# Optimization experiments

Hardware: AMD Instinct MI355X
Metric: run time of the kernel (lower is better)

The kernel has to match this reference:

```python
import jax, jax.numpy as jnp
import numpy as np

B, N, D, R, W, H, I = 256, 2048, 128, 4, 1, 1024, 1024
CI = I + R * D                       # controller input size (1536)
IF = 2 * D * W + 2 * W + 1 + 4 * R + D * R   # interface size (787)
OPI = H + R * D                      # output_proj input (1536)


def _norm(v):
    # F.normalize(dim=-1): x / max(||x||, eps)
    return v / jnp.maximum(jnp.linalg.norm(v, axis=-1, keepdims=True), 1e-12)


def setup_inputs() -> dict:
    key = jax.random.key(0)
    ks = jax.random.split(key, 16)
    u = lambda k, shape, fan: jax.random.uniform(k, shape, jnp.float32, -1.0 / np.sqrt(fan), 1.0 / np.sqrt(fan))
    return {
        "x": jax.random.normal(ks[0], (B, I), jnp.float32),
        "memory": jax.random.normal(ks[1], (N, D), jnp.float32) * np.sqrt(2.0 / (N + D)),  # xavier-ish
        "usage": jax.random.uniform(ks[2], (N,), jnp.float32),          # usage in [0,1)
        "link": jax.random.normal(ks[3], (N, N), jnp.float32) * 0.01,   # non-trivial link state
        "W_ih": u(ks[4], (4 * H, CI), H),
        "W_hh": u(ks[5], (4 * H, H), H),
        "b_ih": u(ks[6], (4 * H,), H),
        "b_hh": u(ks[7], (4 * H,), H),
        "W_if": u(ks[8], (IF, H), H),
        "b_if": u(ks[9], (IF,), H),
        "W_out": u(ks[10], (H, OPI), OPI),
        "b_out": u(ks[11], (H,), OPI),
    }


def reference(x, memory, usage, link, W_ih, W_hh, b_ih, b_hh, W_if, b_if, W_out, b_out):
    # initial uniform read weights (prev state at first step)
    prev_rw = jnp.full((B, R, N), 1.0 / N, x.dtype)
    read_flat = (prev_rw @ memory).reshape(B, -1)                 # (B, R*D)
    cin = jnp.concatenate([x, read_flat], axis=-1)                # (B, CI)

    # single LSTM step, h0 = c0 = 0, torch gate order i,f,g,o
    g = cin @ W_ih.T + b_ih + b_hh
    gi, gf, gg, go = jnp.split(g, 4, axis=-1)
    c = jax.nn.sigmoid(gi) * jnp.tanh(gg)
    h = jax.nn.sigmoid(go) * jnp.tanh(c)                          # (B, H) controller out

    itf = h @ W_if.T + b_if                                       # (B, IF)
    o = 0
    write_vals = itf[:, o:o + D * W].reshape(B, W, D); o += D * W
    erase = jax.nn.sigmoid(itf[:, o:o + D * W]).reshape(B, W, D); o += D * W
    write_gates = jax.nn.sigmoid(itf[:, o:o + W]); o += W         # (B, W)
    alloc_gate = jax.nn.sigmoid(itf[:, o:o + 1]); o += 1          # (B, 1)
    o += W                                                        # free gates (parsed, unused)
    read_modes = jax.nn.softmax(itf[:, o:o + 3 * R].reshape(B, R, 3), -1); o += 3 * R
    read_str = jax.nn.softplus(itf[:, o:o + R]); o += R           # (B, R)
    read_keys = itf[:, o:o + D * R].reshape(B, R, D)

    # content addressing for the write (strength = 1)
    mem_n = _norm(memory)
    cw = jax.nn.softmax(_norm(write_vals.mean(1)) @ mem_n.T, -1)  # (B, N)

    # allocation weighting: sorted-usage cumprod (per source semantics)
    idx = jnp.argsort(usage)
    su = usage[idx]
    cp = jnp.cumprod(1.0 - su)
    alloc_s = jnp.concatenate([su[:1], su[1:] * cp[:-1]])
    alloc = jnp.zeros_like(usage).at[idx].set(alloc_s)[None, :] * alloc_gate  # (B, N)

    write_w = write_gates[:, :, None] * (0.5 * cw + 0.5 * alloc)[:, None, :]  # (B, W, N)

    # temporal link update: batch-mean of diag-masked outer product, decay 0.9
    lu = jnp.einsum('bwn,bwm->nm', write_w, write_w) / B
    lu = lu * (1.0 - jnp.eye(N, dtype=lu.dtype))
    link_new = link * 0.9 + lu * 0.1

    # memory write (erase then add, batch-mean)
    ev = erase * write_gates[:, :, None]
    av = write_vals * write_gates[:, :, None]
    erase_mat = jnp.einsum('bwn,bwd->nd', write_w, ev) / B
    add_mat = jnp.einsum('bwn,bwd->nd', write_w, av) / B
    mem_new = memory * (1.0 - erase_mat) + add_mat

    # read addressing on updated memory and updated link (all R heads vectorized)
    sim = jnp.einsum('brd,nd->brn', _norm(read_keys), _norm(mem_new))
    content_r = jax.nn.softmax(sim * read_str[:, :, None], -1)    # (B, R, N)
    backward_w = jnp.einsum('brn,nm->brm', prev_rw, link_new)     # mode 1: prev @ L
    forward_w = jnp.einsum('brn,mn->brm', prev_rw, link_new)      # mode 2: prev @ L^T
    new_rw = (read_modes[..., 0:1] * content_r
              + read_modes[..., 1:2] * backward_w
              + read_modes[..., 2:3] * forward_w)                 # (B, R, N)

    read_out = (new_rw @ mem_new).reshape(B, -1)                  # (B, R*D)
    out = jnp.concatenate([h, read_out], axis=-1) @ W_out.T + b_out
    return out
```

## Files before the change

### kernel.cpp

```cpp
#include <hip/hip_runtime.h>
#include <cmath>

#define DEVI __device__ __forceinline__

DEVI float sigm(float x){ return 1.f/(1.f+expf(-x)); }

typedef __attribute__((ext_vector_type(8))) _Float16 half8;
typedef __attribute__((ext_vector_type(4))) _Float16 half4;
typedef __attribute__((ext_vector_type(4))) float float4v;


__global__ void k_zero(float* __restrict__ p, int n){
  int i = blockIdx.x*256 + threadIdx.x;
  if (i < n) p[i] = 0.f;
}

__global__ __launch_bounds__(256) void k_stage1(
    const float* __restrict__ mem, float* __restrict__ cm, _Float16* __restrict__ mem_h)
{
  __shared__ float smem[4][132];
  const int blk = blockIdx.x, t = threadIdx.x;
  const int wv = t >> 6, lane = t & 63;
  int rbase = blk*16 + wv*4;
  float x0[4], x1[4], ss[4];
  #pragma unroll
  for (int u = 0; u < 4; u++){
    const float* a = mem + (size_t)(rbase+u)*128;
    x0[u] = a[lane]; x1[u] = a[lane+64];
  }
  #pragma unroll
  for (int u = 0; u < 4; u++) ss[u] = x0[u]*x0[u] + x1[u]*x1[u];
  #pragma unroll
  for (int o = 1; o < 64; o <<= 1){
    #pragma unroll
    for (int u = 0; u < 4; u++) ss[u] += __shfl_xor(ss[u], o);
  }
  float c0 = 0.f, c1 = 0.f;
  #pragma unroll
  for (int u = 0; u < 4; u++){
    float invn = 1.f / fmaxf(sqrtf(ss[u]), 1e-12f);
    mem_h[(size_t)(rbase+u)*128 + lane]      = (_Float16)(x0[u]*invn);
    mem_h[(size_t)(rbase+u)*128 + 64 + lane] = (_Float16)(x1[u]*invn);
    c0 += x0[u]; c1 += x1[u];
  }
  smem[wv][lane] = c0; smem[wv][64+lane] = c1;
  __syncthreads();
  if (t < 128) atomicAdd(&cm[t], smem[0][t]+smem[1][t]+smem[2][t]+smem[3][t]);
}

#define QA 264
#define QB 520
#define QB3 776

template<typename TB> struct BReg;
template<> struct BReg<_Float16>{
  half8 v;
  DEVI void load(const _Float16* p){ v = *(const half8*)p; }
  DEVI half8 get() const { return v; }
};
template<> struct BReg<float>{
  float4v a, b;
  DEVI void load(const float* p){ a = *(const float4v*)p; b = *(const float4v*)(p+4); }
  DEVI half8 get() const {
    half8 h;
    #pragma unroll
    for (int j = 0; j < 4; j++){ h[j] = (_Float16)a[j]; h[4+j] = (_Float16)b[j]; }
    return h;
  }
};

struct ARegX {
  float4v a, b; float sc;
  DEVI void load(const float* __restrict__ x, const float* __restrict__ cm, int row, int k){
    const float* p;
    if (k < 1024){ p = x + (size_t)row*1024 + k; sc = 1.f; }
    else         { p = cm + ((k - 1024) & 127); sc = (1.f/2048.f); }
    a = *(const float4v*)p; b = *(const float4v*)(p+4);
  }
  DEVI half8 get() const {
    half8 h;
    #pragma unroll
    for (int j = 0; j < 4; j++){ h[j] = (_Float16)(a[j]*sc); h[4+j] = (_Float16)(b[j]*sc); }
    return h;
  }
};

template<typename TB>
__global__ __launch_bounds__(256) void gemm_t(
    const _Float16* __restrict__ A, const TB* __restrict__ Bm, float* __restrict__ C,
    int M, int N, int K,
    const float* __restrict__ bias1, const float* __restrict__ bias2)
{
  __shared__ _Float16 Ah[2][8*QA];
  __shared__ _Float16 Bh[2][8*QB];
  const int tid = threadIdx.x;
  const int m0 = blockIdx.y*32, n0 = blockIdx.x*64;
  const int T = K >> 6;
  const int arow = tid >> 3, aq = tid & 7;
  const int brow = tid >> 3, bq = tid & 7;
  int nB0 = n0 + brow;      if (nB0 >= N) nB0 = N - 1;
  int nB1 = n0 + brow + 32; if (nB1 >= N) nB1 = N - 1;
  const _Float16* Aptr = A + (size_t)(m0 + arow)*K + aq*8;
  const TB* Bp0 = Bm + (size_t)nB0*K + bq*8;
  const TB* Bp1 = Bm + (size_t)nB1*K + bq*8;
  const int wA  = aq*QA + arow*8;
  const int wB0 = bq*QB + brow*8;
  const int wB1 = bq*QB + (brow+32)*8;
  const int wv_ = tid >> 6, lane = tid & 63;
  const int fq = lane >> 4, fr = lane & 15;
  const int m16 = (wv_ & 1)*16, nb = (wv_ >> 1)*32;

  half8 ra0, ra1;
  BReg<TB> rb00, rb10, rb01, rb11;
  ra0 = *(const half8*)(Aptr);
  rb00.load(Bp0); rb10.load(Bp1);
  if (T > 1){
    ra1 = *(const half8*)(Aptr + 64);
    rb01.load(Bp0 + 64); rb11.load(Bp1 + 64);
  }
  *(half8*)&Ah[0][wA]  = ra0;
  *(half8*)&Bh[0][wB0] = rb00.get();
  *(half8*)&Bh[0][wB1] = rb10.get();
  __syncthreads();

  float4v acc0 = {0.f,0.f,0.f,0.f}, acc1 = {0.f,0.f,0.f,0.f};
  for (int t = 0; t < T; t++){
    const int cur = t & 1, nxt = cur ^ 1;
    if (t+2 < T){
      if (cur == 0){
        ra0 = *(const half8*)(Aptr + (t+2)*64);
        rb00.load(Bp0 + (t+2)*64); rb10.load(Bp1 + (t+2)*64);
      } else {
        ra1 = *(const half8*)(Aptr + (t+2)*64);
        rb01.load(Bp0 + (t+2)*64); rb11.load(Bp1 + (t+2)*64);
      }
    }
    #pragma unroll
    for (int s = 0; s < 2; s++){
      int q = s*4 + fq;
      half8 a  = *(half8*)&Ah[cur][q*QA + (m16+fr)*8];
      half8 b0 = *(half8*)&Bh[cur][q*QB + (nb+fr)*8];
      half8 b1 = *(half8*)&Bh[cur][q*QB + (nb+16+fr)*8];
      acc0 = __builtin_amdgcn_mfma_f32_16x16x32_f16(a, b0, acc0, 0, 0, 0);
      acc1 = __builtin_amdgcn_mfma_f32_16x16x32_f16(a, b1, acc1, 0, 0, 0);
    }
    if (t+1 < T){
      if (nxt == 1){
        *(half8*)&Ah[1][wA]  = ra1;
        *(half8*)&Bh[1][wB0] = rb01.get();
        *(half8*)&Bh[1][wB1] = rb11.get();
      } else {
        *(half8*)&Ah[0][wA]  = ra0;
        *(half8*)&Bh[0][wB0] = rb00.get();
        *(half8*)&Bh[0][wB1] = rb10.get();
      }
    }
    __syncthreads();
  }

  const int colA = n0 + nb + fr, colB = colA + 16;
  #pragma unroll
  for (int i = 0; i < 4; i++){
    int m = m0 + m16 + fq*4 + i;
    if (colA < N){
      float v = acc0[i];
      if (bias1) v += bias1[colA];
      if (bias2) v += bias2[colA];
      C[(size_t)m*N + colA] = v;
    }
    if (colB < N){
      float v = acc1[i];
      if (bias1) v += bias1[colB];
      if (bias2) v += bias2[colB];
      C[(size_t)m*N + colB] = v;
    }
  }
}

__global__ __launch_bounds__(256) void gemm_hro(
    const _Float16* __restrict__ Ah_, const _Float16* __restrict__ Aro,
    const float* __restrict__ Bm, float* __restrict__ C,
    const float* __restrict__ bias1)
{
  __shared__ _Float16 Ah[2][8*QA];
  __shared__ _Float16 Bh[2][8*QB];
  const int tid = threadIdx.x;
  const int m0 = blockIdx.y*32, n0 = blockIdx.x*64;
  const int T = 24;
  const int arow = tid >> 3, aq = tid & 7;
  const int brow = tid >> 3, bq = tid & 7;
  const int arw = m0 + arow;
  const float* Bp0 = Bm + (size_t)(n0 + brow)*1536 + bq*8;
  const float* Bp1 = Bm + (size_t)(n0 + brow + 32)*1536 + bq*8;
  const int wA  = aq*QA + arow*8;
  const int wB0 = bq*QB + brow*8;
  const int wB1 = bq*QB + (brow+32)*8;
  const int wv_ = tid >> 6, lane = tid & 63;
  const int fq = lane >> 4, fr = lane & 15;
  const int m16 = (wv_ & 1)*16, nb = (wv_ >> 1)*32;

  auto ldA = [&](int k) -> half8 {
    const _Float16* p = (k < 1024) ? (Ah_ + (size_t)arw*1024 + k)
                                   : (Aro + (size_t)arw*512 + (k - 1024));
    return *(const half8*)p;
  };

  half8 ra0, ra1;
  BReg<float> rb00, rb10, rb01, rb11;
  ra0 = ldA(aq*8);
  rb00.load(Bp0); rb10.load(Bp1);
  ra1 = ldA(aq*8 + 64);
  rb01.load(Bp0 + 64); rb11.load(Bp1 + 64);
  *(half8*)&Ah[0][wA]  = ra0;
  *(half8*)&Bh[0][wB0] = rb00.get();
  *(half8*)&Bh[0][wB1] = rb10.get();
  __syncthreads();

  float4v acc0 = {0.f,0.f,0.f,0.f}, acc1 = {0.f,0.f,0.f,0.f};
  for (int t = 0; t < T; t++){
    const int cur = t & 1, nxt = cur ^ 1;
    if (t+2 < T){
      if (cur == 0){
        ra0 = ldA(aq*8 + (t+2)*64);
        rb00.load(Bp0 + (t+2)*64); rb10.load(Bp1 + (t+2)*64);
      } else {
        ra1 = ldA(aq*8 + (t+2)*64);
        rb01.load(Bp0 + (t+2)*64); rb11.load(Bp1 + (t+2)*64);
      }
    }
    #pragma unroll
    for (int s = 0; s < 2; s++){
      int q = s*4 + fq;
      half8 a  = *(half8*)&Ah[cur][q*QA + (m16+fr)*8];
      half8 b0 = *(half8*)&Bh[cur][q*QB + (nb+fr)*8];
      half8 b1 = *(half8*)&Bh[cur][q*QB + (nb+16+fr)*8];
      acc0 = __builtin_amdgcn_mfma_f32_16x16x32_f16(a, b0, acc0, 0, 0, 0);
      acc1 = __builtin_amdgcn_mfma_f32_16x16x32_f16(a, b1, acc1, 0, 0, 0);
    }
    if (t+1 < T){
      if (nxt == 1){
        *(half8*)&Ah[1][wA]  = ra1;
        *(half8*)&Bh[1][wB0] = rb01.get();
        *(half8*)&Bh[1][wB1] = rb11.get();
      } else {
        *(half8*)&Ah[0][wA]  = ra0;
        *(half8*)&Bh[0][wB0] = rb00.get();
        *(half8*)&Bh[0][wB1] = rb10.get();
      }
    }
    __syncthreads();
  }

  const int colA = n0 + nb + fr, colB = colA + 16;
  #pragma unroll
  for (int i = 0; i < 4; i++){
    int m = m0 + m16 + fq*4 + i;
    C[(size_t)m*1024 + colA] = acc0[i] + bias1[colA];
    C[(size_t)m*1024 + colB] = acc1[i] + bias1[colB];
  }
}

__global__ __launch_bounds__(256) void k_gemm_wwExp(
    const _Float16* __restrict__ A, const _Float16* __restrict__ Bm,
    float* __restrict__ C, float* __restrict__ rsum)
{
  __shared__ _Float16 Ah[2][8*QA];
  __shared__ _Float16 Bh[2][8*QB];
  const int tid = threadIdx.x;
  const int m0 = blockIdx.y*32, n0 = blockIdx.x*64;
  const int arow = tid >> 3, aq = tid & 7;
  const int brow = tid >> 3, bq = tid & 7;
  const _Float16* Aptr = A + (size_t)(m0 + arow)*128 + aq*8;
  const _Float16* Bp0 = Bm + (size_t)(n0 + brow)*128 + bq*8;
  const _Float16* Bp1 = Bm + (size_t)(n0 + brow + 32)*128 + bq*8;
  const int wA  = aq*QA + arow*8;
  const int wB0 = bq*QB + brow*8;
  const int wB1 = bq*QB + (brow+32)*8;
  const int wv_ = tid >> 6, lane = tid & 63;
  const int fq = lane >> 4, fr = lane & 15;
  const int m16 = (wv_ & 1)*16, nb = (wv_ >> 1)*32;

  half8 ra  = *(const half8*)(Aptr);
  half8 rb0 = *(const half8*)(Bp0);
  half8 rb1 = *(const half8*)(Bp1);
  *(half8*)&Ah[0][wA]  = ra;
  *(half8*)&Bh[0][wB0] = rb0;
  *(half8*)&Bh[0][wB1] = rb1;
  __syncthreads();

  float4v acc0 = {0.f,0.f,0.f,0.f}, acc1 = {0.f,0.f,0.f,0.f};
  for (int t = 0; t < 2; t++){
    const int cur = t & 1, nxt = cur ^ 1;
    if (t == 0){
      ra  = *(const half8*)(Aptr + 64);
      rb0 = *(const half8*)(Bp0 + 64);
      rb1 = *(const half8*)(Bp1 + 64);
    }
    #pragma unroll
    for (int s = 0; s < 2; s++){
      int q = s*4 + fq;
      half8 a  = *(half8*)&Ah[cur][q*QA + (m16+fr)*8];
      half8 b0 = *(half8*)&Bh[cur][q*QB + (nb+fr)*8];
      half8 b1 = *(half8*)&Bh[cur][q*QB + (nb+16+fr)*8];
      acc0 = __builtin_amdgcn_mfma_f32_16x16x32_f16(a, b0, acc0, 0, 0, 0);
      acc1 = __builtin_amdgcn_mfma_f32_16x16x32_f16(a, b1, acc1, 0, 0, 0);
    }
    if (t == 0){
      *(half8*)&Ah[nxt][wA]  = ra;
      *(half8*)&Bh[nxt][wB0] = rb0;
      *(half8*)&Bh[nxt][wB1] = rb1;
    }
    __syncthreads();
  }

  const int colA = n0 + nb + fr, colB = colA + 16;
  #pragma unroll
  for (int i = 0; i < 4; i++){
    int m = m0 + m16 + fq*4 + i;
    float e0 = expf(acc0[i]);
    float e1 = expf(acc1[i]);
    C[(size_t)m*2048 + colA] = e0;
    C[(size_t)m*2048 + colB] = e1;
    float rs = e0 + e1;
    #pragma unroll
    for (int o = 1; o < 16; o <<= 1) rs += __shfl_xor(rs, o);
    if (fr == 0) atomicAdd(&rsum[m], rs);
  }
}

__global__ __launch_bounds__(256) void k_big2(
    const float* __restrict__ x, const float* __restrict__ cm,
    const float* __restrict__ W,
    const float* __restrict__ b_ih, const float* __restrict__ b_hh,
    _Float16* __restrict__ h,
    const float* __restrict__ usage, float* __restrict__ alloc,
    const float* __restrict__ link, float* __restrict__ rsl, float* __restrict__ cslp)
{
  extern __shared__ char smraw[];
  const int blk = blockIdx.x, tid = threadIdx.x;
  const int wv = tid >> 6, lane = tid & 63;

  if (blk < 256){
    _Float16* AhP = (_Float16*)smraw;
    _Float16* BhP = (_Float16*)(smraw + 2*8*QA*sizeof(_Float16));
    const int SA = 8*QA, SB = 8*QB3;
    const int m0 = (blk >> 5)*32, c0 = (blk & 31)*32;
    const int T = 24;
    const int arow = tid >> 3, aq = tid & 7;
    const int brow = tid >> 3, bq = tid & 7;
    const int arw = m0 + arow;
    const float* Bpi = W + (size_t)(       c0 + brow)*1536 + bq*8;
    const float* Bpg = W + (size_t)(2048 + c0 + brow)*1536 + bq*8;
    const float* Bpo = W + (size_t)(3072 + c0 + brow)*1536 + bq*8;
    const int wA  = aq*QA + arow*8;
    const int wBi = bq*QB3 + brow*8;
    const int wBg = bq*QB3 + (32+brow)*8;
    const int wBo = bq*QB3 + (64+brow)*8;
    const int fq = lane >> 4, fr = lane & 15;
    const int m16 = (wv & 1)*16, c16 = (wv >> 1)*16;

    ARegX ax0, ax1;
    BReg<float> ri0, rg0, ro0, ri1, rg1, ro1;
    ax0.load(x, cm, arw, aq*8);
    ri0.load(Bpi); rg0.load(Bpg); ro0.load(Bpo);
    ax1.load(x, cm, arw, aq*8 + 64);
    ri1.load(Bpi + 64); rg1.load(Bpg + 64); ro1.load(Bpo + 64);
    *(half8*)&AhP[wA]  = ax0.get();
    *(half8*)&BhP[wBi] = ri0.get();
    *(half8*)&BhP[wBg] = rg0.get();
    *(half8*)&BhP[wBo] = ro0.get();
    __syncthreads();

    float4v acci = {0.f,0.f,0.f,0.f}, accg = {0.f,0.f,0.f,0.f}, acco = {0.f,0.f,0.f,0.f};
    for (int t = 0; t < T; t++){
      const int cur = t & 1, nxt = cur ^ 1;
      if (t+2 < T){
        if (cur == 0){
          ax0.load(x, cm, arw, aq*8 + (t+2)*64);
          ri0.load(Bpi + (t+2)*64); rg0.load(Bpg + (t+2)*64); ro0.load(Bpo + (t+2)*64);
        } else {
          ax1.load(x, cm, arw, aq*8 + (t+2)*64);
          ri1.load(Bpi + (t+2)*64); rg1.load(Bpg + (t+2)*64); ro1.load(Bpo + (t+2)*64);
        }
      }
      #pragma unroll
      for (int s = 0; s < 2; s++){
        int q = s*4 + fq;
        half8 a  = *(half8*)&AhP[cur*SA + q*QA + (m16+fr)*8];
        half8 bi = *(half8*)&BhP[cur*SB + q*QB3 + (c16+fr)*8];
        half8 bg = *(half8*)&BhP[cur*SB + q*QB3 + (32+c16+fr)*8];
        half8 bo = *(half8*)&BhP[cur*SB + q*QB3 + (64+c16+fr)*8];
        acci = __builtin_amdgcn_mfma_f32_16x16x32_f16(a, bi, acci, 0, 0, 0);
        accg = __builtin_amdgcn_mfma_f32_16x16x32_f16(a, bg, accg, 0, 0, 0);
        acco = __builtin_amdgcn_mfma_f32_16x16x32_f16(a, bo, acco, 0, 0, 0);
      }
      if (t+1 < T){
        if (nxt == 1){
          *(half8*)&AhP[SA + wA]  = ax1.get();
          *(half8*)&BhP[SB + wBi] = ri1.get();
          *(half8*)&BhP[SB + wBg] = rg1.get();
          *(half8*)&BhP[SB + wBo] = ro1.get();
        } else {
          *(half8*)&AhP[wA]  = ax0.get();
          *(half8*)&BhP[wBi] = ri0.get();
          *(half8*)&BhP[wBg] = rg0.get();
          *(half8*)&BhP[wBo] = ro0.get();
        }
      }
      __syncthreads();
    }

    const int col = c0 + c16 + fr;
    const float bi1 = b_ih[col]        + b_hh[col];
    const float bg1 = b_ih[2048 + col] + b_hh[2048 + col];
    const float bo1 = b_ih[3072 + col] + b_hh[3072 + col];
    #pragma unroll
    for (int i = 0; i < 4; i++){
      int m = m0 + m16 + fq*4 + i;
      float gi = acci[i] + bi1;
      float gg = accg[i] + bg1;
      float go = acco[i] + bo1;
      float c = sigm(gi) * tanhf(gg);
      h[(size_t)m*1024 + col] = (_Float16)(sigm(go) * tanhf(c));
    }
  } else if (blk < 512){
    float (*smem)[132] = (float(*)[132])smraw;
    int pb = blk - 256;
    int r0 = pb*8;
    int c0 = tid*8;
    float4v v0[8], v1[8];
    #pragma unroll
    for (int u = 0; u < 8; u++){
      const float* lp = link + (size_t)(r0+u)*2048 + c0;
      v0[u] = *(const float4v*)lp;
      v1[u] = *(const float4v*)(lp+4);
    }
    float colacc[8];
    #pragma unroll
    for (int j = 0; j < 8; j++) colacc[j] = 0.f;
    float rowpart[8];
    #pragma unroll
    for (int u = 0; u < 8; u++){
      float s = 0.f;
      #pragma unroll
      for (int j = 0; j < 4; j++){
        colacc[j]   += v0[u][j]; colacc[4+j] += v1[u][j];
        s += v0[u][j] + v1[u][j];
      }
      rowpart[u] = s;
    }
    #pragma unroll
    for (int o = 1; o < 64; o <<= 1){
      #pragma unroll
      for (int u = 0; u < 8; u++) rowpart[u] += __shfl_xor(rowpart[u], o);
    }
    if (lane == 0){
      #pragma unroll
      for (int u = 0; u < 8; u++) smem[wv][u] = rowpart[u];
    }
    __syncthreads();
    if (tid < 8) rsl[r0+tid] = smem[0][tid]+smem[1][tid]+smem[2][tid]+smem[3][tid];
    float4v w0, w1;
    #pragma unroll
    for (int j = 0; j < 4; j++){ w0[j] = colacc[j]; w1[j] = colacc[4+j]; }
    *(float4v*)&cslp[(size_t)pb*2048 + c0]     = w0;
    *(float4v*)&cslp[(size_t)pb*2048 + c0 + 4] = w1;
  } else {
    int n = (blk - 512)*4 + wv;
    float un = usage[n];
    float prod = 1.f;
    #pragma unroll
    for (int i = 0; i < 32; i++){
      int m = lane + i*64;
      float um = usage[m];
      bool before = (um < un) || (um == un && m < n);
      prod *= before ? (1.f - um) : 1.f;
    }
    #pragma unroll
    for (int o = 32; o > 0; o >>= 1) prod *= __shfl_xor(prod, o);
    if (lane == 0) alloc[n] = un * prod;
  }
}

DEVI float blockReduce128(float v, float* lds2){
  #pragma unroll
  for (int o = 32; o > 0; o >>= 1) v += __shfl_xor(v, o);
  int w = threadIdx.x >> 6;
  __syncthreads();
  if ((threadIdx.x & 63) == 0) lds2[w] = v;
  __syncthreads();
  return lds2[0] + lds2[1];
}

__global__ __launch_bounds__(128) void k_parse(const float* __restrict__ itf,
    _Float16* __restrict__ wv_h, float* __restrict__ ev, float* __restrict__ av,
    float* __restrict__ wg_, float* __restrict__ ag_,
    float* __restrict__ rm0, float* __restrict__ rm1, float* __restrict__ rm2,
    _Float16* __restrict__ rks_h)
{
  __shared__ float red[2];
  int b = blockIdx.x, t = threadIdx.x;
  const float* it = itf + (size_t)b*787;
  float wg = sigm(it[256]);
  float ag = sigm(it[257]);
  if (t == 0){ wg_[b] = wg; ag_[b] = ag; }
  float w = it[t];
  av[b*128 + t] = w * wg;
  ev[b*128 + t] = sigm(it[128 + t]) * wg;
  float ss = blockReduce128(w*w, red);
  float invwv = 1.f / fmaxf(sqrtf(ss), 1e-12f);
  wv_h[b*128 + t] = (_Float16)(w * invwv);
  if (t < 4){
    int rr = t;
    float m0v = it[259 + rr*3 + 0], m1v = it[259 + rr*3 + 1], m2v = it[259 + rr*3 + 2];
    float mx = fmaxf(m0v, fmaxf(m1v, m2v));
    float e0 = expf(m0v - mx), e1 = expf(m1v - mx), e2 = expf(m2v - mx);
    float inv = 1.f / (e0 + e1 + e2);
    rm0[b*4 + rr] = e0*inv; rm1[b*4 + rr] = e1*inv; rm2[b*4 + rr] = e2*inv;
  }
  #pragma unroll
  for (int rr = 0; rr < 4; rr++){
    float kv = it[275 + rr*128 + t];
    float ks = blockReduce128(kv*kv, red);
    float sx = it[271 + rr];
    float str = fmaxf(sx, 0.f) + log1pf(expf(-fabsf(sx)));
    float invk = 1.f / fmaxf(sqrtf(ks), 1e-12f);
    rks_h[((size_t)b*4 + rr)*128 + t] = (_Float16)(kv * invk * str);
  }
}

__global__ __launch_bounds__(256) void k_memupdate_fused(const float* __restrict__ ww,
    const float* __restrict__ ev, const float* __restrict__ av,
    const float* __restrict__ mem,
    const float* __restrict__ wg, const float* __restrict__ ag,
    const float* __restrict__ alloc, const float* __restrict__ rsum,
    const float* __restrict__ rsl, const float* __restrict__ cslp,
    _Float16* __restrict__ memn_h, _Float16* __restrict__ memnT_h,
    float* __restrict__ bwm, float* __restrict__ fwm)
{
  __shared__ float Ws[16][34];
  __shared__ float Es[16][132], Vs[16][132];
  __shared__ float lb[128], lf[128];
  __shared__ _Float16 Traw[32][132];
  __shared__ float tbs[256], c1s[256], c2s[256];
  __shared__ float allocL[32];
  __shared__ float sq[8][32], sd[8][32];
  __shared__ float cpart[8][32];
  __shared__ float bwL[32], fwL[32];
  __shared__ float sred[4];
  const int n0 = blockIdx.x*32;
  const int tid = threadIdx.x, tx = tid & 31, ty = tid >> 5;

  {
    float sa = 0.f;
    #pragma unroll
    for (int i = 0; i < 8; i++) sa += alloc[tid + i*256];
    #pragma unroll
    for (int o = 32; o > 0; o >>= 1) sa += __shfl_xor(sa, o);
    if ((tid & 63) == 0) sred[tid >> 6] = sa;
    if (tid < 128){ lb[tid] = 0.f; lf[tid] = 0.f; }
    if (tid < 32) allocL[tid] = alloc[n0 + tid];
    __syncthreads();
    sa = (sred[0]+sred[1]) + (sred[2]+sred[3]);
    float w = wg[tid], a = ag[tid];
    tbs[tid] = w*(0.5f + 0.5f*a*sa);
    c1s[tid] = 0.5f*w / rsum[tid];
    c2s[tid] = 0.5f*w*a;
  }
  {
    int col = n0 + tx;
    float s = 0.f;
    for (int p = ty*32; p < ty*32 + 32; p += 4){
      s += cslp[(size_t)(p+0)*2048 + col] + cslp[(size_t)(p+1)*2048 + col]
         + cslp[(size_t)(p+2)*2048 + col] + cslp[(size_t)(p+3)*2048 + col];
    }
    cpart[ty][tx] = s;
  }
  __syncthreads();

  const int wk = tid >> 4, wn = (tid & 15)*2;
  const int ek = tid >> 4, ec = (tid & 15)*8;
  float ae[4][4] = {}, aa[4][4] = {};
  float qp = 0.f, ddp = 0.f;
  for (int k0 = 0; k0 < 256; k0 += 16){
    float2 vw  = *(const float2*)(ww + (size_t)(k0+wk)*2048 + n0 + wn);
    float4 ve0 = *(const float4*)(ev + (size_t)(k0+ek)*128 + ec);
    float4 ve1 = *(const float4*)(ev + (size_t)(k0+ek)*128 + ec + 4);
    float4 va0 = *(const float4*)(av + (size_t)(k0+ek)*128 + ec);
    float4 va1 = *(const float4*)(av + (size_t)(k0+ek)*128 + ec + 4);
    __syncthreads();
    {
      float cb1 = c1s[k0+wk], cb2 = c2s[k0+wk];
      Ws[wk][wn]   = cb1*vw.x + cb2*allocL[wn];
      Ws[wk][wn+1] = cb1*vw.y + cb2*allocL[wn+1];
    }
    *(float4*)&Es[ek][ec] = ve0; *(float4*)&Es[ek][ec+4] = ve1;
    *(float4*)&Vs[ek][ec] = va0; *(float4*)&Vs[ek][ec+4] = va1;
    __syncthreads();
    #pragma unroll
    for (int k = 0; k < 16; k++){
      float a[4], e[4], v[4];
      #pragma unroll
      for (int i = 0; i < 4; i++) a[i] = Ws[k][ty*4+i];
      #pragma unroll
      for (int j = 0; j < 4; j++){ e[j] = Es[k][tx*4+j]; v[j] = Vs[k][tx*4+j]; }
      #pragma unroll
      for (int i = 0; i < 4; i++)
        #pragma unroll
        for (int j = 0; j < 4; j++){
          ae[i][j] = fmaf(a[i], e[j], ae[i][j]);
          aa[i][j] = fmaf(a[i], v[j], aa[i][j]);
        }
    }
    {
      float w0 = Ws[ty*2+0][tx], w1 = Ws[ty*2+1][tx];
      qp  = fmaf(tbs[k0+ty*2+0], w0, qp);  ddp = fmaf(w0, w0, ddp);
      qp  = fmaf(tbs[k0+ty*2+1], w1, qp);  ddp = fmaf(w1, w1, ddp);
    }
  }
  sq[ty][tx] = qp; sd[ty][tx] = ddp;
  __syncthreads();
  if (tid < 32){
    float q = 0.f, dd = 0.f, cs = 0.f;
    #pragma unroll
    for (int z = 0; z < 8; z++){ q += sq[z][tid]; dd += sd[z][tid]; cs += cpart[z][tid]; }
    float lus = (q - dd) * (1.f/256.f);
    bwL[tid] = (0.9f*cs + 0.1f*lus) * (1.f/2048.f);
    fwL[tid] = (0.9f*rsl[n0+tid] + 0.1f*lus) * (1.f/2048.f);
  }
  __syncthreads();

  float ab[4] = {0,0,0,0}, af[4] = {0,0,0,0};
  #pragma unroll
  for (int i = 0; i < 4; i++){
    int n = n0 + ty*4 + i;
    float bwn = bwL[ty*4+i], fwn = fwL[ty*4+i];
    float v[4]; float ss = 0.f;
    #pragma unroll
    for (int j = 0; j < 4; j++){
      int d = tx*4 + j;
      float em = ae[i][j]*(1.f/256.f), am = aa[i][j]*(1.f/256.f);
      float mv = mem[(size_t)n*128 + d]*(1.f - em) + am;
      v[j] = mv; ss += mv*mv;
      ab[j] = fmaf(bwn, mv, ab[j]);
      af[j] = fmaf(fwn, mv, af[j]);
    }
    #pragma unroll
    for (int o = 1; o < 32; o <<= 1) ss += __shfl_xor(ss, o);
    float invn = 1.f / fmaxf(sqrtf(ss), 1e-12f);
    half4 hn, hr;
    #pragma unroll
    for (int j = 0; j < 4; j++){ hn[j] = (_Float16)(v[j]*invn); hr[j] = (_Float16)v[j]; }
    *(half4*)(memn_h + (size_t)n*128 + tx*4) = hn;
    *(half4*)&Traw[ty*4+i][tx*4] = hr;
  }
  __syncthreads();
  {
    int d = tid >> 1, seg = (tid & 1)*16;
    half8 o0, o1;
    #pragma unroll
    for (int j = 0; j < 8; j++){ o0[j] = Traw[seg+j][d]; o1[j] = Traw[seg+8+j][d]; }
    *(half8*)(memnT_h + (size_t)d*2048 + n0 + seg)     = o0;
    *(half8*)(memnT_h + (size_t)d*2048 + n0 + seg + 8) = o1;
  }
  #pragma unroll
  for (int j = 0; j < 4; j++){
    atomicAdd(&lb[tx*4+j], ab[j]);
    atomicAdd(&lf[tx*4+j], af[j]);
  }
  __syncthreads();
  if (tid < 128){
    atomicAdd(&bwm[tid], lb[tid]);
    atomicAdd(&fwm[tid], lf[tid]);
  }
}

__global__ __launch_bounds__(256) void k_flash(
    const _Float16* __restrict__ Q, const _Float16* __restrict__ Kh,
    const _Float16* __restrict__ Vt,
    float* __restrict__ pacc, float* __restrict__ pm, float* __restrict__ pl)
{
  __shared__ _Float16 Pl[4][16][32];
  __shared__ float cmb[4][2080];
  __shared__ float scl[4][16];
  const int tid = threadIdx.x;
  const int qt = blockIdx.x >> 3, kc = blockIdx.x & 7;
  const int wv = tid >> 6, lane = tid & 63;
  const int fq = lane >> 4, fr = lane & 15;
  const int kw0 = kc*256 + wv*64;

  half8 aq[4];
  #pragma unroll
  for (int c = 0; c < 4; c++)
    aq[c] = *(const half8*)(Q + (size_t)(qt*16 + fr)*128 + c*32 + fq*8);

  float m[4] = {-3.0e38f,-3.0e38f,-3.0e38f,-3.0e38f};
  float l[4] = {0.f,0.f,0.f,0.f};
  float4v acc[8] = {};
  for (int s = 0; s < 2; s++){
    const int kb = kw0 + s*32;
    float4v S0 = {0,0,0,0}, S1 = {0,0,0,0};
    #pragma unroll
    for (int c = 0; c < 4; c++){
      half8 b0 = *(const half8*)(Kh + (size_t)(kb + fr)*128      + c*32 + fq*8);
      half8 b1 = *(const half8*)(Kh + (size_t)(kb + 16 + fr)*128 + c*32 + fq*8);
      S0 = __builtin_amdgcn_mfma_f32_16x16x32_f16(aq[c], b0, S0, 0, 0, 0);
      S1 = __builtin_amdgcn_mfma_f32_16x16x32_f16(aq[c], b1, S1, 0, 0, 0);
    }
    float mt[4], ps[4];
    #pragma unroll
    for (int i = 0; i < 4; i++) mt[i] = fmaxf(S0[i], S1[i]);
    #pragma unroll
    for (int o = 1; o < 16; o <<= 1){
      #pragma unroll
      for (int i = 0; i < 4; i++) mt[i] = fmaxf(mt[i], __shfl_xor(mt[i], o));
    }
    #pragma unroll
    for (int i = 0; i < 4; i++){
      float mn = fmaxf(m[i], mt[i]);
      float al = expf(m[i] - mn);
      float p0 = expf(S0[i] - mn), p1 = expf(S1[i] - mn);
      S0[i] = p0; S1[i] = p1;
      ps[i] = p0 + p1;
      l[i] *= al;
      m[i] = mn;
      #pragma unroll
      for (int c = 0; c < 8; c++) acc[c][i] *= al;
    }
    #pragma unroll
    for (int o = 1; o < 16; o <<= 1){
      #pragma unroll
      for (int i = 0; i < 4; i++) ps[i] += __shfl_xor(ps[i], o);
    }
    #pragma unroll
    for (int i = 0; i < 4; i++) l[i] += ps[i];
    #pragma unroll
    for (int i = 0; i < 4; i++){
      Pl[wv][fq*4+i][fr]      = (_Float16)S0[i];
      Pl[wv][fq*4+i][16 + fr] = (_Float16)S1[i];
    }
    half8 pf = *(half8*)&Pl[wv][fr][fq*8];
    #pragma unroll
    for (int c = 0; c < 8; c++){
      half8 bv = *(const half8*)(Vt + (size_t)(c*16 + fr)*2048 + kb + fq*8);
      acc[c] = __builtin_amdgcn_mfma_f32_16x16x32_f16(pf, bv, acc[c], 0, 0, 0);
    }
  }
  if (fr == 0){
    #pragma unroll
    for (int i = 0; i < 4; i++){
      cmb[wv][fq*4+i]      = m[i];
      cmb[wv][16 + fq*4+i] = l[i];
    }
  }
  #pragma unroll
  for (int c = 0; c < 8; c++)
    #pragma unroll
    for (int i = 0; i < 4; i++)
      cmb[wv][32 + (fq*4+i)*128 + c*16 + fr] = acc[c][i];
  __syncthreads();
  if (tid < 16){
    float mm = fmaxf(fmaxf(cmb[0][tid], cmb[1][tid]), fmaxf(cmb[2][tid], cmb[3][tid]));
    float ll = 0.f;
    #pragma unroll
    for (int w = 0; w < 4; w++){
      float e = expf(cmb[w][tid] - mm);
      scl[w][tid] = e;
      ll += e * cmb[w][16 + tid];
    }
    pm[blockIdx.x*16 + tid] = mm;
    pl[blockIdx.x*16 + tid] = ll;
  }
  __syncthreads();
  for (int e = tid; e < 2048; e += 256){
    int q = e >> 7;
    float a = scl[0][q]*cmb[0][32+e] + scl[1][q]*cmb[1][32+e]
            + scl[2][q]*cmb[2][32+e] + scl[3][q]*cmb[3][32+e];
    pacc[(size_t)blockIdx.x*2048 + e] = a;
  }
}

__global__ void k_ro(const float* __restrict__ pacc, const float* __restrict__ pm,
                     const float* __restrict__ pl,
                     const float* __restrict__ rm0, const float* __restrict__ rm1,
                     const float* __restrict__ rm2, const float* __restrict__ bwm,
                     const float* __restrict__ fwm, _Float16* __restrict__ ro){
  int idx = blockIdx.x*256 + threadIdx.x;
  int row = idx >> 7, d = idx & 127;
  int qt = row >> 4, q = row & 15;
  float mm = -3.0e38f;
  #pragma unroll
  for (int kc = 0; kc < 8; kc++) mm = fmaxf(mm, pm[(qt*8+kc)*16 + q]);
  float num = 0.f, den = 0.f;
  #pragma unroll
  for (int kc = 0; kc < 8; kc++){
    float e = expf(pm[(qt*8+kc)*16 + q] - mm);
    den += e * pl[(qt*8+kc)*16 + q];
    num += e * pacc[(size_t)(qt*8+kc)*2048 + q*128 + d];
  }
  float pv = num / den;
  ro[idx] = (_Float16)(rm0[row]*pv + rm1[row]*bwm[d] + rm2[row]*fwm[d]);
}


extern "C" void kernel_launch(void* const* d_in, const int* in_sizes, int n_in,
                              void* d_out, int out_size, void* d_ws, size_t ws_size,
                              hipStream_t stream)
{
  const float* x     = (const float*)d_in[0];
  const float* mem   = (const float*)d_in[1];
  const float* usage = (const float*)d_in[2];
  const float* link  = (const float*)d_in[3];
  const float* W_ih  = (const float*)d_in[4];
  const float* b_ih  = (const float*)d_in[6];
  const float* b_hh  = (const float*)d_in[7];
  const float* W_if  = (const float*)d_in[8];
  const float* b_if  = (const float*)d_in[9];
  const float* W_out = (const float*)d_in[10];
  const float* b_out = (const float*)d_in[11];
  float* out = (float*)d_out;
  float* ws  = (float*)d_ws;

  float* cm     = ws + 0;
  float* bwm    = ws + 2176;
  float* fwm    = ws + 2304;
  float* rsum   = ws + 2432;
  float* wg     = ws + 6784;
  float* ag     = ws + 7040;
  float* rm0    = ws + 7296;
  float* rm1    = ws + 8320;
  float* rm2    = ws + 9344;
  float* alloc  = ws + 10368;
  float* rsl    = ws + 12416;
  float* ev     = ws + 14464;
  float* av     = ws + 47232;
  float* itf    = ws + 1128576;
  float* ww     = ws + 1330048;
  float* pacc   = ws + 1854336;
  float* pm     = ws + 2902912;
  float* pl     = ws + 2911104;
  _Float16* wv_h    = (_Float16*)(ws + 2919296);
  _Float16* mem_h   = (_Float16*)(ws + 2935680);
  _Float16* memn_h  = (_Float16*)(ws + 3066752);
  _Float16* memnT_h = (_Float16*)(ws + 3197824);
  _Float16* rks_h   = (_Float16*)(ws + 3328896);
  _Float16* ro_h    = (_Float16*)(ws + 3394432);
  _Float16* h_h     = (_Float16*)(ws + 3459968);
  float* cslp       = ws + 3591040;

  const int SH_BIG2 = (2*8*QA + 2*8*QB3) * (int)sizeof(_Float16);

  k_zero<<<11, 256, 0, stream>>>(ws, 2688);

  k_stage1<<<128, 256, 0, stream>>>(mem, cm, mem_h);

  k_big2<<<1024, 256, SH_BIG2, stream>>>(x, cm, W_ih, b_ih, b_hh, h_h,
                                         usage, alloc, link, rsl, cslp);

  gemm_t<float><<<dim3(13,8), 256, 0, stream>>>(h_h, W_if, itf, 256, 787, 1024, b_if, nullptr);
  k_parse<<<256, 128, 0, stream>>>(itf, wv_h, ev, av, wg, ag, rm0, rm1, rm2, rks_h);

  k_gemm_wwExp<<<dim3(32,8), 256, 0, stream>>>(wv_h, mem_h, ww, rsum);

  k_memupdate_fused<<<64, 256, 0, stream>>>(ww, ev, av, mem, wg, ag, alloc, rsum,
                                            rsl, cslp, memn_h, memnT_h, bwm, fwm);

  k_flash<<<512, 256, 0, stream>>>(rks_h, memn_h, memnT_h, pacc, pm, pl);

  k_ro<<<512, 256, 0, stream>>>(pacc, pm, pl, rm0, rm1, rm2, bwm, fwm, ro_h);
  gemm_hro<<<dim3(16,8), 256, 0, stream>>>(h_h, ro_h, W_out, out, b_out);

  (void)in_sizes; (void)n_in; (void)out_size; (void)ws_size;
}
```

Measured before the change: 230.1 us.

## Restructure memory-update kernel to 8 rows per block with direct loads

The fused memory-update kernel now gives each block 8 memory rows instead of 32 and launches 256 blocks instead of 64. Each thread handles one row and four columns and streams the write-weight, erase and add vectors straight from global memory, replacing the shared-memory tiled outer product and its per-tile barriers. The goal is more parallelism across the GPU and fewer synchronisations. In exchange, each block rereads the erase and add matrices, so cache traffic rises and there are four times as many global atomics into bwm and fwm.

```diff
diff --git a/kernel.cpp b/kernel.cpp
--- a/kernel.cpp
+++ b/kernel.cpp
@@ -538,140 +538,98 @@
     _Float16* __restrict__ memn_h, _Float16* __restrict__ memnT_h,
     float* __restrict__ bwm, float* __restrict__ fwm)
 {
-  __shared__ float Ws[16][34];
-  __shared__ float Es[16][132], Vs[16][132];
+  __shared__ float ccs[256][4];
   __shared__ float lb[128], lf[128];
-  __shared__ _Float16 Traw[32][132];
-  __shared__ float tbs[256], c1s[256], c2s[256];
-  __shared__ float allocL[32];
-  __shared__ float sq[8][32], sd[8][32];
-  __shared__ float cpart[8][32];
-  __shared__ float bwL[32], fwL[32];
+  __shared__ _Float16 Traw[8][136];
+  __shared__ float cpartS[8];
   __shared__ float sred[4];
-  const int n0 = blockIdx.x*32;
-  const int tid = threadIdx.x, tx = tid & 31, ty = tid >> 5;
-
+  const int n0 = blockIdx.x*8;
+  const int tid = threadIdx.x;
+  const int nl = tid >> 5, dq = tid & 31;
+  const int n = n0 + nl;
+
+  if (tid < 128){ lb[tid] = 0.f; lf[tid] = 0.f; }
+  float sa = 0.f;
+  #pragma unroll
+  for (int i = 0; i < 8; i++) sa += alloc[tid + i*256];
+  #pragma unroll
+  for (int o = 32; o > 0; o >>= 1) sa += __shfl_xor(sa, o);
+  if ((tid & 63) == 0) sred[tid >> 6] = sa;
+  float cp = 0.f;
   {
-    float sa = 0.f;
-    #pragma unroll
-    for (int i = 0; i < 8; i++) sa += alloc[tid + i*256];
-    #pragma unroll
-    for (int o = 32; o > 0; o >>= 1) sa += __shfl_xor(sa, o);
-    if ((tid & 63) == 0) sred[tid >> 6] = sa;
-    if (tid < 128){ lb[tid] = 0.f; lf[tid] = 0.f; }
-    if (tid < 32) allocL[tid] = alloc[n0 + tid];
-    __syncthreads();
-    sa = (sred[0]+sred[1]) + (sred[2]+sred[3]);
+    const float* cb = cslp + (size_t)(dq*8)*2048 + n;
+    #pragma unroll
+    for (int p = 0; p < 8; p++) cp += cb[(size_t)p*2048];
+    #pragma unroll
+    for (int o = 1; o < 32; o <<= 1) cp += __shfl_xor(cp, o);
+  }
+  const float aln = alloc[n];
+  __syncthreads();
+  sa = (sred[0]+sred[1]) + (sred[2]+sred[3]);
+  {
     float w = wg[tid], a = ag[tid];
-    tbs[tid] = w*(0.5f + 0.5f*a*sa);
-    c1s[tid] = 0.5f*w / rsum[tid];
-    c2s[tid] = 0.5f*w*a;
-  }
-  {
-    int col = n0 + tx;
-    float s = 0.f;
-    for (int p = ty*32; p < ty*32 + 32; p += 4){
-      s += cslp[(size_t)(p+0)*2048 + col] + cslp[(size_t)(p+1)*2048 + col]
-         + cslp[(size_t)(p+2)*2048 + col] + cslp[(size_t)(p+3)*2048 + col];
-    }
-    cpart[ty][tx] = s;
-  }
-  __syncthreads();
-
-  const int wk = tid >> 4, wn = (tid & 15)*2;
-  const int ek = tid >> 4, ec = (tid & 15)*8;
-  float ae[4][4] = {}, aa[4][4] = {};
+    ccs[tid][0] = 0.5f*w / rsum[tid];
+    ccs[tid][1] = 0.5f*w*a;
+    ccs[tid][2] = w*(0.5f + 0.5f*a*sa);
+    ccs[tid][3] = 0.f;
+  }
+  if (dq == 0) cpartS[nl] = cp;
+  __syncthreads();
+
+  float ae[4] = {0.f,0.f,0.f,0.f}, aa[4] = {0.f,0.f,0.f,0.f};
   float qp = 0.f, ddp = 0.f;
-  for (int k0 = 0; k0 < 256; k0 += 16){
-    float2 vw  = *(const float2*)(ww + (size_t)(k0+wk)*2048 + n0 + wn);
-    float4 ve0 = *(const float4*)(ev + (size_t)(k0+ek)*128 + ec);
-    float4 ve1 = *(const float4*)(ev + (size_t)(k0+ek)*128 + ec + 4);
-    float4 va0 = *(const float4*)(av + (size_t)(k0+ek)*128 + ec);
-    float4 va1 = *(const float4*)(av + (size_t)(k0+ek)*128 + ec + 4);
-    __syncthreads();
-    {
-      float cb1 = c1s[k0+wk], cb2 = c2s[k0+wk];
-      Ws[wk][wn]   = cb1*vw.x + cb2*allocL[wn];
-      Ws[wk][wn+1] = cb1*vw.y + cb2*allocL[wn+1];
-    }
-    *(float4*)&Es[ek][ec] = ve0; *(float4*)&Es[ek][ec+4] = ve1;
-    *(float4*)&Vs[ek][ec] = va0; *(float4*)&Vs[ek][ec+4] = va1;
-    __syncthreads();
-    #pragma unroll
-    for (int k = 0; k < 16; k++){
-      float a[4], e[4], v[4];
-      #pragma unroll
-      for (int i = 0; i < 4; i++) a[i] = Ws[k][ty*4+i];
-      #pragma unroll
-      for (int j = 0; j < 4; j++){ e[j] = Es[k][tx*4+j]; v[j] = Vs[k][tx*4+j]; }
-      #pragma unroll
-      for (int i = 0; i < 4; i++)
-        #pragma unroll
-        for (int j = 0; j < 4; j++){
-          ae[i][j] = fmaf(a[i], e[j], ae[i][j]);
-          aa[i][j] = fmaf(a[i], v[j], aa[i][j]);
-        }
-    }
-    {
-      float w0 = Ws[ty*2+0][tx], w1 = Ws[ty*2+1][tx];
-      qp  = fmaf(tbs[k0+ty*2+0], w0, qp);  ddp = fmaf(w0, w0, ddp);
-      qp  = fmaf(tbs[k0+ty*2+1], w1, qp);  ddp = fmaf(w1, w1, ddp);
-    }
-  }
-  sq[ty][tx] = qp; sd[ty][tx] = ddp;
-  __syncthreads();
-  if (tid < 32){
-    float q = 0.f, dd = 0.f, cs = 0.f;
-    #pragma unroll
-    for (int z = 0; z < 8; z++){ q += sq[z][tid]; dd += sd[z][tid]; cs += cpart[z][tid]; }
-    float lus = (q - dd) * (1.f/256.f);
-    bwL[tid] = (0.9f*cs + 0.1f*lus) * (1.f/2048.f);
-    fwL[tid] = (0.9f*rsl[n0+tid] + 0.1f*lus) * (1.f/2048.f);
-  }
-  __syncthreads();
-
-  float ab[4] = {0,0,0,0}, af[4] = {0,0,0,0};
-  #pragma unroll
-  for (int i = 0; i < 4; i++){
-    int n = n0 + ty*4 + i;
-    float bwn = bwL[ty*4+i], fwn = fwL[ty*4+i];
-    float v[4]; float ss = 0.f;
+  #pragma unroll 4
+  for (int k = 0; k < 256; k++){
+    float4v cc = *(const float4v*)&ccs[k][0];
+    float we = ww[(size_t)k*2048 + n];
+    float4v e4 = *(const float4v*)(ev + (size_t)k*128 + dq*4);
+    float4v v4 = *(const float4v*)(av + (size_t)k*128 + dq*4);
+    float w = cc[0]*we + cc[1]*aln;
     #pragma unroll
     for (int j = 0; j < 4; j++){
-      int d = tx*4 + j;
-      float em = ae[i][j]*(1.f/256.f), am = aa[i][j]*(1.f/256.f);
-      float mv = mem[(size_t)n*128 + d]*(1.f - em) + am;
-      v[j] = mv; ss += mv*mv;
-      ab[j] = fmaf(bwn, mv, ab[j]);
-      af[j] = fmaf(fwn, mv, af[j]);
-    }
-    #pragma unroll
-    for (int o = 1; o < 32; o <<= 1) ss += __shfl_xor(ss, o);
-    float invn = 1.f / fmaxf(sqrtf(ss), 1e-12f);
-    half4 hn, hr;
-    #pragma unroll
-    for (int j = 0; j < 4; j++){ hn[j] = (_Float16)(v[j]*invn); hr[j] = (_Float16)v[j]; }
-    *(half4*)(memn_h + (size_t)n*128 + tx*4) = hn;
-    *(half4*)&Traw[ty*4+i][tx*4] = hr;
-  }
-  __syncthreads();
-  {
-    int d = tid >> 1, seg = (tid & 1)*16;
-    half8 o0, o1;
-    #pragma unroll
-    for (int j = 0; j < 8; j++){ o0[j] = Traw[seg+j][d]; o1[j] = Traw[seg+8+j][d]; }
-    *(half8*)(memnT_h + (size_t)d*2048 + n0 + seg)     = o0;
-    *(half8*)(memnT_h + (size_t)d*2048 + n0 + seg + 8) = o1;
-  }
+      ae[j] = fmaf(w, e4[j], ae[j]);
+      aa[j] = fmaf(w, v4[j], aa[j]);
+    }
+    qp  = fmaf(cc[2], w, qp);
+    ddp = fmaf(w, w, ddp);
+  }
+
+  float lus = (qp - ddp) * (1.f/256.f);
+  float bwv = (0.9f*cpartS[nl] + 0.1f*lus) * (1.f/2048.f);
+  float fwv = (0.9f*rsl[n]     + 0.1f*lus) * (1.f/2048.f);
+
+  float4v m4 = *(const float4v*)(mem + (size_t)n*128 + dq*4);
+  float v[4]; float ss = 0.f;
+  float ab[4], af[4];
   #pragma unroll
   for (int j = 0; j < 4; j++){
-    atomicAdd(&lb[tx*4+j], ab[j]);
-    atomicAdd(&lf[tx*4+j], af[j]);
+    float em = ae[j]*(1.f/256.f), am = aa[j]*(1.f/256.f);
+    float mv = m4[j]*(1.f - em) + am;
+    v[j] = mv; ss += mv*mv;
+    ab[j] = bwv*mv; af[j] = fwv*mv;
+  }
+  #pragma unroll
+  for (int o = 1; o < 32; o <<= 1) ss += __shfl_xor(ss, o);
+  float invn = 1.f / fmaxf(sqrtf(ss), 1e-12f);
+  half4 hn, hr;
+  #pragma unroll
+  for (int j = 0; j < 4; j++){ hn[j] = (_Float16)(v[j]*invn); hr[j] = (_Float16)v[j]; }
+  *(half4*)(memn_h + (size_t)n*128 + dq*4) = hn;
+  *(half4*)&Traw[nl][dq*4] = hr;
+  #pragma unroll
+  for (int j = 0; j < 4; j++){
+    atomicAdd(&lb[dq*4+j], ab[j]);
+    atomicAdd(&lf[dq*4+j], af[j]);
   }
   __syncthreads();
   if (tid < 128){
-    atomicAdd(&bwm[tid], lb[tid]);
-    atomicAdd(&fwm[tid], lf[tid]);
+    int d = tid;
+    half8 o;
+    #pragma unroll
+    for (int u = 0; u < 8; u++) o[u] = Traw[u][d];
+    *(half8*)(memnT_h + (size_t)d*2048 + n0) = o;
+    atomicAdd(&bwm[d], lb[d]);
+    atomicAdd(&fwm[d], lf[d]);
   }
 }
 
@@ -862,8 +820,8 @@
 
   k_gemm_wwExp<<<dim3(32,8), 256, 0, stream>>>(wv_h, mem_h, ww, rsum);
 
-  k_memupdate_fused<<<64, 256, 0, stream>>>(ww, ev, av, mem, wg, ag, alloc, rsum,
-                                            rsl, cslp, memn_h, memnT_h, bwm, fwm);
+  k_memupdate_fused<<<256, 256, 0, stream>>>(ww, ev, av, mem, wg, ag, alloc, rsum,
+                                             rsl, cslp, memn_h, memnT_h, bwm, fwm);
 
   k_flash<<<512, 256, 0, stream>>>(rks_h, memn_h, memnT_h, pacc, pm, pl);
 
```

New measurement: 271.1 us. 1.18x slower.
